# Optimization experiments

Hardware: AMD Instinct MI355X
Metric: run time of the kernel (lower is better)

The kernel has to match this reference:

```python
import jax, jax.numpy as jnp
import numpy as np

N, E = 50000, 800000
IN_FEAT = OUT_FEAT = 128
EMB = 3
K = 3  # k_order + 1
BN_EPS = 1e-5


def setup_inputs() -> dict:
    key = jax.random.key(0)
    ks = jax.random.split(key, 12)
    feature = jax.random.normal(ks[0], (N, IN_FEAT), jnp.float32)
    coords = jax.random.normal(ks[1], (N, EMB), jnp.float32)
    src = jax.random.randint(ks[2], (E,), 0, N, jnp.int32)
    dst = jax.random.randint(ks[3], (E,), 0, N, jnp.int32)
    order = jax.random.randint(ks[4], (E,), 0, K, jnp.int32)
    # xavier_normal_ on [K, in, out]: torch treats last two dims as (fan_in, fan_out)
    std_lin = float(np.sqrt(2.0 / (IN_FEAT + OUT_FEAT)))
    linear = jax.random.normal(ks[5], (K, IN_FEAT, OUT_FEAT), jnp.float32) * std_lin
    # attention_layer: Linear(EMB, OUT_FEAT, bias=False); store as [EMB, OUT_FEAT]
    lim_att = float(1.0 / np.sqrt(EMB))
    attW = jax.random.uniform(ks[6], (EMB, OUT_FEAT), jnp.float32, -lim_att, lim_att)
    lim_mlp = float(1.0 / np.sqrt(OUT_FEAT))
    mlp_w = jax.random.uniform(ks[7], (OUT_FEAT, OUT_FEAT), jnp.float32, -lim_mlp, lim_mlp)
    mlp_b = jax.random.uniform(ks[8], (OUT_FEAT,), jnp.float32, -lim_mlp, lim_mlp)
    bn_gamma = jnp.ones((OUT_FEAT,), jnp.float32)
    bn_beta = jnp.zeros((OUT_FEAT,), jnp.float32)
    return {"feature": feature, "coords": coords, "src": src, "dst": dst,
            "order": order, "linear": linear, "attW": attW,
            "mlp_w": mlp_w, "mlp_b": mlp_b, "bn_gamma": bn_gamma, "bn_beta": bn_beta}


def reference(feature, coords, src, dst, order, linear, attW, mlp_w, mlp_b, bn_gamma, bn_beta):
    n = feature.shape[0]
    # --- edge attention: dot(attention_layer(c_src - c_dst), h_src) ---
    dc = coords[src] - coords[dst]                      # [E, EMB]
    att = jnp.sum((dc @ attW) * feature[src], axis=1)   # [E]
    invdist = 1.0 / (jnp.sum(dc * dc, axis=1) + 1.0)    # [E], 1/(||dc||^2 + 1)
    # --- messages: per-edge weight selection linear[order] @ h_src ---
    # msg depends only on (src node, order): precompute per-order node transforms
    xk = jnp.einsum('ni,kio->kno', feature, linear)     # [K, N, OUT]
    msg = xk[order, src]                                # [E, OUT]
    # --- segment softmax over incoming edges of dst ---
    m = jax.ops.segment_max(att, dst, num_segments=n)   # [N]
    ex = jnp.exp(att - m[dst])                          # [E]
    denom = jax.ops.segment_sum(ex, dst, num_segments=n)
    d_g = denom[dst]
    alpha = ex / jnp.where(d_g > 0, d_g, 1.0)
    # --- weighted scatter-add aggregation ---
    w = (alpha * invdist)[:, None]                      # [E, 1]
    h = jax.ops.segment_sum(w * msg, dst, num_segments=n)  # [N, OUT]
    # --- mlp: Linear -> ReLU -> BatchNorm1d (training-mode batch stats) ---
    y = jax.nn.relu(h @ mlp_w.T + mlp_b)
    mean = jnp.mean(y, axis=0)
    var = jnp.var(y, axis=0)  # biased, matches torch BN normalization
    y = (y - mean) * jax.lax.rsqrt(var + BN_EPS) * bn_gamma + bn_beta
    return y
```

## Files before the change

kernel.cpp:

```cpp
#include <hip/hip_runtime.h>

#define N_NODES 50000
#define E_EDGES 800000
#define FEAT    128
#define KORD    3
#define BN_EPS  1e-5f
#define NB1     49
#define NBUK    49
#define BCAP    20480
#define NSHARD  16
#define NSEG    32
#define NWB_BLKS 12500
#define NZERO   54368

typedef __fp16 f16x2 __attribute__((ext_vector_type(2)));
typedef __fp16 f16x8 __attribute__((ext_vector_type(8)));
typedef __attribute__((ext_vector_type(4))) float f32x4;

__device__ __forceinline__ unsigned h2u(f16x2 h) { union { f16x2 h; unsigned u; } c; c.h = h; return c.u; }
__device__ __forceinline__ f16x2 u2h(unsigned u) { union { unsigned u; f16x2 h; } c; c.u = u; return c.h; }

__device__ __forceinline__ void gload16(const void* g, void* l) {
    __builtin_amdgcn_global_load_lds(
        (const __attribute__((address_space(1))) unsigned int*)g,
        (__attribute__((address_space(3))) unsigned int*)l, 16, 0, 0);
}

__global__ void g_cast(const float* __restrict__ feat,
                       const float* __restrict__ coords,
                       const float* __restrict__ attW,
                       const float* __restrict__ W,
                       const float* __restrict__ L,
                       __fp16* __restrict__ fh,
                       float4* __restrict__ pk,
                       __fp16* __restrict__ GT,
                       int* __restrict__ zbase) {
    __shared__ float wrow[FEAT];
    const int gtid = blockIdx.x * 256 + threadIdx.x;
    if (gtid < NZERO) zbase[gtid] = 0;
    if (blockIdx.x >= NWB_BLKS) {
        const int o = blockIdx.x - NWB_BLKS;
        const int i = threadIdx.x;
        if (i < FEAT) wrow[i] = W[o * FEAT + i];
        __syncthreads();
        if (i < FEAT) {
            #pragma unroll
            for (int k = 0; k < KORD; ++k) {
                const float* lp = L + ((size_t)k * FEAT + i) * FEAT;
                float acc = 0.f;
                #pragma unroll 8
                for (int j = 0; j < FEAT; ++j) acc = fmaf(lp[j], wrow[j], acc);
                GT[(size_t)o * 384 + k * FEAT + i] = (__fp16)acc;
            }
        }
        return;
    }
    const int node = gtid >> 6;
    const int lane = threadIdx.x & 63;
    if (node >= N_NODES) return;
    const float2 f = *(const float2*)(feat + (size_t)node * FEAT + lane * 2);
    *(f16x2*)(fh + (size_t)node * FEAT + lane * 2) = __builtin_amdgcn_cvt_pkrtz(f.x, f.y);
    float gg[3];
    #pragma unroll
    for (int j = 0; j < 3; ++j) {
        float p = f.x * attW[j * FEAT + lane * 2] + f.y * attW[j * FEAT + lane * 2 + 1];
        #pragma unroll
        for (int off = 32; off; off >>= 1) p += __shfl_xor(p, off);
        gg[j] = p;
    }
    if (lane == 0) {
        const float c0 = coords[node * 3 + 0], c1 = coords[node * 3 + 1], c2 = coords[node * 3 + 2];
        pk[2 * node]     = make_float4(c0, c1, c2, gg[0]);
        pk[2 * node + 1] = make_float4(gg[1], gg[2], 0.f, 0.f);
    }
}

__global__ __launch_bounds__(256)
void bucketA(const int* __restrict__ src, const int* __restrict__ dst,
             const int* __restrict__ order,
             int* __restrict__ cnt, int* __restrict__ gcur, int2* __restrict__ bbuf) {
    __shared__ int lcnt[4][NBUK];
    __shared__ int wbase[4][NBUK];
    const int tid = threadIdx.x;
    const int wid = tid >> 6;
    if (tid < NBUK) {
        lcnt[0][tid] = 0; lcnt[1][tid] = 0; lcnt[2][tid] = 0; lcnt[3][tid] = 0;
    }
    __syncthreads();
    const int e0 = blockIdx.x * 2048;
    int b[8], r[8], so[8], dd[8];
    #pragma unroll
    for (int i = 0; i < 8; ++i) {
        const int e = e0 + i * 256 + tid;
        if (e < E_EDGES) {
            dd[i] = dst[e];
            so[i] = (order[e] << 16) | src[e];
            b[i] = dd[i] >> 10;
            r[i] = atomicAdd(&lcnt[wid][b[i]], 1);
            atomicAdd(cnt + dd[i], 1);
        } else b[i] = -1;
    }
    __syncthreads();
    if (tid < NBUK) {
        const int w0 = lcnt[0][tid], w1 = lcnt[1][tid], w2 = lcnt[2][tid], w3 = lcnt[3][tid];
        const int base = atomicAdd(gcur + tid, w0 + w1 + w2 + w3);
        wbase[0][tid] = base;
        wbase[1][tid] = base + w0;
        wbase[2][tid] = base + w0 + w1;
        wbase[3][tid] = base + w0 + w1 + w2;
    }
    __syncthreads();
    #pragma unroll
    for (int i = 0; i < 8; ++i)
        if (b[i] >= 0)
            bbuf[(size_t)b[i] * BCAP + wbase[wid][b[i]] + r[i]] = make_int2(so[i], dd[i]);
}

__global__ __launch_bounds__(256)
void scan1(const int* __restrict__ cnt, int* __restrict__ rowptr, int* __restrict__ bsum) {
    __shared__ int lds[256];
    const int b = blockIdx.x, t = threadIdx.x;
    const int base = b * 1024 + t * 4;
    int v[4];
    #pragma unroll
    for (int i = 0; i < 4; ++i) v[i] = (base + i < N_NODES) ? cnt[base + i] : 0;
    lds[t] = v[0] + v[1] + v[2] + v[3];
    __syncthreads();
    for (int off = 1; off < 256; off <<= 1) {
        const int u = (t >= off) ? lds[t - off] : 0;
        __syncthreads();
        lds[t] += u;
        __syncthreads();
    }
    int excl = t ? lds[t - 1] : 0;
    if (t == 255) bsum[b] = lds[255];
    #pragma unroll
    for (int i = 0; i < 4; ++i) {
        if (base + i < N_NODES) rowptr[base + i] = excl;
        excl += v[i];
    }
}

__global__ void scan3(int* __restrict__ rowptr, int* __restrict__ cursor,
                      const int* __restrict__ bsum) {
    __shared__ int boff_s[64];
    const int t = threadIdx.x;
    if (t < 64) {
        const int v = (t < NB1) ? bsum[t] : 0;
        int incl = v;
        #pragma unroll
        for (int off = 1; off < 64; off <<= 1) {
            const int u = __shfl_up(incl, off);
            if (t >= off) incl += u;
        }
        boff_s[t] = incl - v;
    }
    __syncthreads();
    const int i = blockIdx.x * 256 + t;
    if (i < N_NODES) {
        const int v = rowptr[i] + boff_s[i >> 10];
        rowptr[i] = v;
        cursor[i] = v;
    }
    if (i == 0) rowptr[N_NODES] = E_EDGES;
}

__global__ void bucketB(const int* __restrict__ gcur, const int2* __restrict__ bbuf,
                        const float4* __restrict__ pk,
                        int* __restrict__ cursor, int4* __restrict__ edata) {
    const int b = blockIdx.x / NSEG;
    const int seg = blockIdx.x % NSEG;
    const int n = gcur[b];
    const int lo = (int)((long)n * seg / NSEG), hi = (int)((long)n * (seg + 1) / NSEG);
    for (int i = lo + (int)threadIdx.x; i < hi; i += 256) {
        const int2 ent = bbuf[(size_t)b * BCAP + i];
        const int s = ent.x & 0xFFFF;
        const int d = ent.y;
        const float4 a0 = pk[2 * s], a1 = pk[2 * s + 1], c0 = pk[2 * d];
        const float dx = a0.x - c0.x, dy = a0.y - c0.y, dz = a0.z - c0.z;
        const float att  = dx * a0.w + dy * a1.x + dz * a1.y;
        const float invd = 1.f / (dx * dx + dy * dy + dz * dz + 1.f);
        const int pos = atomicAdd(cursor + d, 1);
        edata[pos] = make_int4(ent.x, __float_as_int(att), __float_as_int(invd), 0);
    }
}

__global__ void segagg(const int4* __restrict__ edata,
                       const int* __restrict__ rowptr,
                       const __fp16* __restrict__ fh,
                       __fp16* __restrict__ agg) {
    __shared__ uint4 stash[4][64];
    const int node = (blockIdx.x * blockDim.x + threadIdx.x) >> 6;
    const int lane = threadIdx.x & 63;
    const int wid  = threadIdx.x >> 6;
    if (node >= N_NODES) return;
    const int beg = rowptr[node], end = rowptr[node + 1];

    int4 e0c = make_int4(0, 0xFF800000, 0, 0);
    float m = -1e30f, s = 0.f;
    int nch = 0;
    for (int cb = beg; cb < end; cb += 64, ++nch) {
        const int p = cb + lane;
        float a = -1e30f;
        if (p < end) {
            const int4 e = edata[p];
            a = __int_as_float(e.y);
            if (nch == 0) e0c = e;
        }
        const float mn = fmaxf(m, a);
        s = s * __expf(m - mn) + ((p < end) ? __expf(a - mn) : 0.f);
        m = mn;
    }
    #pragma unroll
    for (int off = 32; off; off >>= 1) {
        const float mo = __shfl_xor(m, off), so_ = __shfl_xor(s, off);
        const float mn = fmaxf(m, mo);
        s = s * __expf(m - mn) + so_ * __expf(mo - mn);
        m = mn;
    }
    const float inv_s = s > 0.f ? 1.f / s : 0.f;

    const int grp = lane >> 4;
    const int fl  = lane & 15;
    f16x2 ac[3][4];
    #pragma unroll
    for (int o = 0; o < 3; ++o)
        #pragma unroll
        for (int q = 0; q < 4; ++q) ac[o][q] = (f16x2){0, 0};

    int ch = 0;
    for (int cb = beg; cb < end; cb += 64, ++ch) {
        const int p = cb + lane;
        float wl = 0.f; int so = 0;
        if (p < end) {
            const int4 e = (ch == 0) ? e0c : edata[p];
            wl = __expf(__int_as_float(e.y) - m) * inv_s * __int_as_float(e.z);
            so = e.x;
        }
        const int k = so >> 16;
        const __fp16 wh = (__fp16)wl;
        f16x2 w2; w2.x = wh; w2.y = wh;
        const unsigned uw = h2u(w2);
        stash[wid][lane] = make_uint4(k == 0 ? uw : 0u, k == 1 ? uw : 0u,
                                      k == 2 ? uw : 0u, (unsigned)(so & 0xFFFF));
        const int ne = min(64, end - cb);
        const uint4* st = stash[wid];
        for (int t = 0; t < ne; t += 8) {
            const uint4 e1 = st[t + grp];
            const uint4 e2 = st[t + 4 + grp];
            const uint4 v1 = *(const uint4*)(fh + ((size_t)e1.w << 7) + fl * 8);
            const uint4 v2 = *(const uint4*)(fh + ((size_t)e2.w << 7) + fl * 8);
            {
                const f16x2 w0 = u2h(e1.x), w1 = u2h(e1.y), w2v = u2h(e1.z);
                const f16x2 va = u2h(v1.x), vb = u2h(v1.y), vc = u2h(v1.z), vd = u2h(v1.w);
                ac[0][0] = __builtin_elementwise_fma(va, w0, ac[0][0]);
                ac[0][1] = __builtin_elementwise_fma(vb, w0, ac[0][1]);
                ac[0][2] = __builtin_elementwise_fma(vc, w0, ac[0][2]);
                ac[0][3] = __builtin_elementwise_fma(vd, w0, ac[0][3]);
                ac[1][0] = __builtin_elementwise_fma(va, w1, ac[1][0]);
                ac[1][1] = __builtin_elementwise_fma(vb, w1, ac[1][1]);
                ac[1][2] = __builtin_elementwise_fma(vc, w1, ac[1][2]);
                ac[1][3] = __builtin_elementwise_fma(vd, w1, ac[1][3]);
                ac[2][0] = __builtin_elementwise_fma(va, w2v, ac[2][0]);
                ac[2][1] = __builtin_elementwise_fma(vb, w2v, ac[2][1]);
                ac[2][2] = __builtin_elementwise_fma(vc, w2v, ac[2][2]);
                ac[2][3] = __builtin_elementwise_fma(vd, w2v, ac[2][3]);
            }
            {
                const f16x2 w0 = u2h(e2.x), w1 = u2h(e2.y), w2v = u2h(e2.z);
                const f16x2 va = u2h(v2.x), vb = u2h(v2.y), vc = u2h(v2.z), vd = u2h(v2.w);
                ac[0][0] = __builtin_elementwise_fma(va, w0, ac[0][0]);
                ac[0][1] = __builtin_elementwise_fma(vb, w0, ac[0][1]);
                ac[0][2] = __builtin_elementwise_fma(vc, w0, ac[0][2]);
                ac[0][3] = __builtin_elementwise_fma(vd, w0, ac[0][3]);
                ac[1][0] = __builtin_elementwise_fma(va, w1, ac[1][0]);
                ac[1][1] = __builtin_elementwise_fma(vb, w1, ac[1][1]);
                ac[1][2] = __builtin_elementwise_fma(vc, w1, ac[1][2]);
                ac[1][3] = __builtin_elementwise_fma(vd, w1, ac[1][3]);
                ac[2][0] = __builtin_elementwise_fma(va, w2v, ac[2][0]);
                ac[2][1] = __builtin_elementwise_fma(vb, w2v, ac[2][1]);
                ac[2][2] = __builtin_elementwise_fma(vc, w2v, ac[2][2]);
                ac[2][3] = __builtin_elementwise_fma(vd, w2v, ac[2][3]);
            }
        }
    }
    #pragma unroll
    for (int o = 0; o < 3; ++o)
        #pragma unroll
        for (int q = 0; q < 4; ++q) {
            ac[o][q] = ac[o][q] + u2h(__shfl_xor((int)h2u(ac[o][q]), 16));
            ac[o][q] = ac[o][q] + u2h(__shfl_xor((int)h2u(ac[o][q]), 32));
        }
    if (lane < 16) {
        __fp16* row = agg + (size_t)node * 384 + fl * 8;
        *(uint4*)(row)       = make_uint4(h2u(ac[0][0]), h2u(ac[0][1]), h2u(ac[0][2]), h2u(ac[0][3]));
        *(uint4*)(row + 128) = make_uint4(h2u(ac[1][0]), h2u(ac[1][1]), h2u(ac[1][2]), h2u(ac[1][3]));
        *(uint4*)(row + 256) = make_uint4(h2u(ac[2][0]), h2u(ac[2][1]), h2u(ac[2][2]), h2u(ac[2][3]));
    }
}

__global__ __launch_bounds__(256)
void mlp_gemm(const __fp16* __restrict__ agg, const __fp16* __restrict__ GT,
              float* __restrict__ out, int M,
              const float* __restrict__ bias, float* __restrict__ sbuf) {
    __shared__ char smem[49152];
    const int m0 = blockIdx.x * 64;
    const int tid = threadIdx.x;
    const int wave = tid >> 6, lane = tid & 63;
    const int wm0 = wave * 16;
    const int lrow = lane & 15;
    const int kg = lane >> 4;
    const int srow = lane >> 3;
    const int schunk = lane & 7;

    auto STAGE = [&](int buf, int kc) {
        char* base = smem + buf * 24576;
        #pragma unroll
        for (int j = 0; j < 2; ++j) {
            const int rl = wave * 16 + j * 8 + srow;
            const int rg = min(m0 + rl, M - 1);
            gload16(agg + (size_t)rg * 384 + kc * 64 + ((schunk ^ (rl & 7)) << 3),
                    base + (wave * 16 + j * 8) * 128);
        }
        #pragma unroll
        for (int j = 0; j < 4; ++j) {
            const int rl = wave * 32 + j * 8 + srow;
            gload16(GT + (size_t)rl * 384 + kc * 64 + ((schunk ^ (rl & 7)) << 3),
                    base + 8192 + (wave * 32 + j * 8) * 128);
        }
    };

    f32x4 acc[8];
    #pragma unroll
    for (int b = 0; b < 8; ++b) acc[b] = (f32x4){0.f, 0.f, 0.f, 0.f};

    STAGE(0, 0);
    __syncthreads();

    for (int kc = 0; kc < 6; ++kc) {
        const int buf = kc & 1;
        if (kc < 5) STAGE(buf ^ 1, kc + 1);
        const char* Ab = smem + buf * 24576;
        const char* Bb = Ab + 8192;
        f16x8 afr[2];
        #pragma unroll
        for (int ks = 0; ks < 2; ++ks) {
            const int row = wm0 + lrow;
            afr[ks] = *(const f16x8*)(Ab + row * 128 + (((ks * 4 + kg) ^ (row & 7)) << 4));
        }
        #pragma unroll
        for (int nf = 0; nf < 8; ++nf) {
            #pragma unroll
            for (int ks = 0; ks < 2; ++ks) {
                const int row = nf * 16 + lrow;
                f16x8 bfr = *(const f16x8*)(Bb + row * 128 + (((ks * 4 + kg) ^ (row & 7)) << 4));
                acc[nf] = __builtin_amdgcn_mfma_f32_16x16x32_f16(afr[ks], bfr, acc[nf], 0, 0, 0);
            }
        }
        __syncthreads();
    }

    float s[8], s2[8], bv[8];
    #pragma unroll
    for (int nf = 0; nf < 8; ++nf) { s[nf] = 0.f; s2[nf] = 0.f; bv[nf] = bias[nf * 16 + lrow]; }
    #pragma unroll
    for (int nf = 0; nf < 8; ++nf)
        #pragma unroll
        for (int rg = 0; rg < 4; ++rg) {
            const int row = m0 + wm0 + kg * 4 + rg;
            if (row < M) {
                const float v = fmaxf(acc[nf][rg] + bv[nf], 0.f);
                out[(size_t)row * FEAT + nf * 16 + lrow] = v;
                s[nf] += v;
                s2[nf] = fmaf(v, v, s2[nf]);
            }
        }
    #pragma unroll
    for (int nf = 0; nf < 8; ++nf) {
        s[nf]  += __shfl_xor(s[nf], 16);  s[nf]  += __shfl_xor(s[nf], 32);
        s2[nf] += __shfl_xor(s2[nf], 16); s2[nf] += __shfl_xor(s2[nf], 32);
    }
    __syncthreads();
    float* red = (float*)smem;
    if (lane < 16) {
        #pragma unroll
        for (int nf = 0; nf < 8; ++nf) {
            red[wave * 256 + nf * 16 + lane]       = s[nf];
            red[wave * 256 + 128 + nf * 16 + lane] = s2[nf];
        }
    }
    __syncthreads();
    if (tid < 128) {
        const float ss = red[tid] + red[256 + tid] + red[512 + tid] + red[768 + tid];
        const float qq = red[128 + tid] + red[384 + tid] + red[640 + tid] + red[896 + tid];
        float* sb = sbuf + (blockIdx.x & (NSHARD - 1)) * 256;
        atomicAdd(sb + tid, ss);
        atomicAdd(sb + FEAT + tid, qq);
    }
}

__global__ void normalize(float* __restrict__ y, const float* __restrict__ sbuf,
                          const float* __restrict__ gamma, const float* __restrict__ beta) {
    __shared__ float sc_s[FEAT], sh_s[FEAT];
    const int t = threadIdx.x;
    if (t < FEAT) {
        float ssum = 0.f, qsum = 0.f;
        #pragma unroll
        for (int sh = 0; sh < NSHARD; ++sh) {
            ssum += sbuf[sh * 256 + t];
            qsum += sbuf[sh * 256 + 128 + t];
        }
        const float mean = ssum / (float)N_NODES;
        const float var  = qsum / (float)N_NODES - mean * mean;
        const float sc   = gamma[t] * rsqrtf(var + BN_EPS);
        sc_s[t] = sc;
        sh_s[t] = beta[t] - mean * sc;
    }
    __syncthreads();
    const int idx = blockIdx.x * blockDim.x + t;
    const int o4 = (idx & 31) * 4;
    float4 v = *(float4*)(y + (size_t)idx * 4);
    const float4 sc = *(const float4*)(sc_s + o4);
    const float4 sh = *(const float4*)(sh_s + o4);
    v.x = fmaf(v.x, sc.x, sh.x);
    v.y = fmaf(v.y, sc.y, sh.y);
    v.z = fmaf(v.z, sc.z, sh.z);
    v.w = fmaf(v.w, sc.w, sh.w);
    *(float4*)(y + (size_t)idx * 4) = v;
}

extern "C" void kernel_launch(void* const* d_in, const int* in_sizes, int n_in,
                              void* d_out, int out_size, void* d_ws, size_t ws_size,
                              hipStream_t stream) {
    const float* feature = (const float*)d_in[0];
    const float* coords  = (const float*)d_in[1];
    const int*   src     = (const int*)d_in[2];
    const int*   dst     = (const int*)d_in[3];
    const int*   order   = (const int*)d_in[4];
    const float* linear  = (const float*)d_in[5];
    const float* attW    = (const float*)d_in[6];
    const float* mlp_w   = (const float*)d_in[7];
    const float* mlp_b   = (const float*)d_in[8];
    const float* gamma   = (const float*)d_in[9];
    const float* beta    = (const float*)d_in[10];
    float* out = (float*)d_out;

    char* p = (char*)d_ws;
    __fp16* fh           = (__fp16*)p;  p += (size_t)N_NODES * FEAT * 2;
    __fp16* agg          = (__fp16*)p;  p += (size_t)N_NODES * 384 * 2;
    __fp16* GT           = (__fp16*)p;  p += (size_t)FEAT * 384 * 2;
    float4* pk           = (float4*)p;  p += (size_t)N_NODES * 32;
    int4*  edata         = (int4*)p;    p += (size_t)E_EDGES * 16;
    int2*  bbuf          = (int2*)p;    p += (size_t)NBUK * BCAP * 8;
    int*   cnt           = (int*)p;     p += 200064;
    float* sbuf          = (float*)p;   p += NSHARD * 256 * 4;
    int*   gcur          = (int*)p;     p += 1024;
    int*   rowptr        = (int*)p;     p += 200064;
    int*   cursor        = (int*)p;     p += 200064;
    int*   bsum          = (int*)p;     p += 256;

    const int MB = (N_NODES + 63) / 64;
    const int AB = (E_EDGES + 2047) / 2048;

    g_cast<<<NWB_BLKS + FEAT, 256, 0, stream>>>(feature, coords, attW,
                                                mlp_w, linear, fh, pk, GT, cnt);

    bucketA<<<AB, 256, 0, stream>>>(src, dst, order, cnt, gcur, bbuf);
    scan1<<<NB1, 256, 0, stream>>>(cnt, rowptr, bsum);
    scan3<<<(N_NODES + 255) / 256, 256, 0, stream>>>(rowptr, cursor, bsum);
    bucketB<<<NBUK * NSEG, 256, 0, stream>>>(gcur, bbuf, pk, cursor, edata);

    segagg<<<NWB_BLKS, 256, 0, stream>>>(edata, rowptr, fh, agg);

    mlp_gemm<<<MB, 256, 0, stream>>>(agg, GT, out, N_NODES, mlp_b, sbuf);
    normalize<<<(N_NODES * 32) / 256, 256, 0, stream>>>(out, sbuf, gamma, beta);
}
```

Baseline: 172.1 us.

## Compute per-node degree histogram from buckets and fuse scans into one kernel

Stops bucketA from issuing a global atomicAdd per edge into a degree array. A new hist2 kernel builds the per-node histogram for each 1024-node bucket in LDS from the already bucketed edges, scans it, and adds the bucket offset taken from a scan over the bucket counts. This replaces two scan kernels and shrinks the zeroing region because the cnt array is gone. The cost is a second read pass over bbuf, and only 49 blocks with heavy LDS atomics, so parallelism in this stage is low.

Result: faster. 162.6 us (-5.5%).

```diff
diff --git a/kernel.cpp b/kernel.cpp
--- a/kernel.cpp
+++ b/kernel.cpp
@@ -5,13 +5,12 @@
 #define FEAT    128
 #define KORD    3
 #define BN_EPS  1e-5f
-#define NB1     49
 #define NBUK    49
 #define BCAP    20480
 #define NSHARD  16
 #define NSEG    32
 #define NWB_BLKS 12500
-#define NZERO   54368
+#define NZERO   4352
 
 typedef __fp16 f16x2 __attribute__((ext_vector_type(2)));
 typedef __fp16 f16x8 __attribute__((ext_vector_type(8)));
@@ -78,7 +77,7 @@
 __global__ __launch_bounds__(256)
 void bucketA(const int* __restrict__ src, const int* __restrict__ dst,
              const int* __restrict__ order,
-             int* __restrict__ cnt, int* __restrict__ gcur, int2* __restrict__ bbuf) {
+             int* __restrict__ gcur, int2* __restrict__ bbuf) {
     __shared__ int lcnt[4][NBUK];
     __shared__ int wbase[4][NBUK];
     const int tid = threadIdx.x;
@@ -97,7 +96,6 @@
             so[i] = (order[e] << 16) | src[e];
             b[i] = dd[i] >> 10;
             r[i] = atomicAdd(&lcnt[wid][b[i]], 1);
-            atomicAdd(cnt + dd[i], 1);
         } else b[i] = -1;
     }
     __syncthreads();
@@ -117,52 +115,50 @@
 }
 
 __global__ __launch_bounds__(256)
-void scan1(const int* __restrict__ cnt, int* __restrict__ rowptr, int* __restrict__ bsum) {
-    __shared__ int lds[256];
-    const int b = blockIdx.x, t = threadIdx.x;
-    const int base = b * 1024 + t * 4;
-    int v[4];
-    #pragma unroll
-    for (int i = 0; i < 4; ++i) v[i] = (base + i < N_NODES) ? cnt[base + i] : 0;
-    lds[t] = v[0] + v[1] + v[2] + v[3];
-    __syncthreads();
-    for (int off = 1; off < 256; off <<= 1) {
-        const int u = (t >= off) ? lds[t - off] : 0;
-        __syncthreads();
-        lds[t] += u;
-        __syncthreads();
-    }
-    int excl = t ? lds[t - 1] : 0;
-    if (t == 255) bsum[b] = lds[255];
-    #pragma unroll
-    for (int i = 0; i < 4; ++i) {
-        if (base + i < N_NODES) rowptr[base + i] = excl;
-        excl += v[i];
-    }
-}
-
-__global__ void scan3(int* __restrict__ rowptr, int* __restrict__ cursor,
-                      const int* __restrict__ bsum) {
-    __shared__ int boff_s[64];
+void hist2(const int* __restrict__ gcur, const int2* __restrict__ bbuf,
+           int* __restrict__ rowptr, int* __restrict__ cursor) {
+    __shared__ int lhist[1024];
+    __shared__ int lscan[256];
+    __shared__ int boff_s;
+    const int b = blockIdx.x;
     const int t = threadIdx.x;
+    #pragma unroll
+    for (int i = 0; i < 4; ++i) lhist[t + i * 256] = 0;
+    __syncthreads();
+    const int n = gcur[b];
+    const int base = b << 10;
+    for (int i = t; i < n; i += 256)
+        atomicAdd(&lhist[bbuf[(size_t)b * BCAP + i].y - base], 1);
+    __syncthreads();
     if (t < 64) {
-        const int v = (t < NB1) ? bsum[t] : 0;
+        const int v = (t < NBUK) ? gcur[t] : 0;
         int incl = v;
         #pragma unroll
         for (int off = 1; off < 64; off <<= 1) {
             const int u = __shfl_up(incl, off);
             if (t >= off) incl += u;
         }
-        boff_s[t] = incl - v;
-    }
-    __syncthreads();
-    const int i = blockIdx.x * 256 + t;
-    if (i < N_NODES) {
-        const int v = rowptr[i] + boff_s[i >> 10];
-        rowptr[i] = v;
-        cursor[i] = v;
-    }
-    if (i == 0) rowptr[N_NODES] = E_EDGES;
+        if (t == b) boff_s = incl - v;
+    }
+    int v[4];
+    #pragma unroll
+    for (int i = 0; i < 4; ++i) v[i] = lhist[t * 4 + i];
+    lscan[t] = v[0] + v[1] + v[2] + v[3];
+    __syncthreads();
+    for (int off = 1; off < 256; off <<= 1) {
+        const int u = (t >= off) ? lscan[t - off] : 0;
+        __syncthreads();
+        lscan[t] += u;
+        __syncthreads();
+    }
+    int excl = (t ? lscan[t - 1] : 0) + boff_s;
+    #pragma unroll
+    for (int i = 0; i < 4; ++i) {
+        const int node = base + t * 4 + i;
+        if (node < N_NODES) { rowptr[node] = excl; cursor[node] = excl; }
+        excl += v[i];
+    }
+    if (b == 0 && t == 0) rowptr[N_NODES] = E_EDGES;
 }
 
 __global__ void bucketB(const int* __restrict__ gcur, const int2* __restrict__ bbuf,
@@ -452,22 +448,19 @@
     float4* pk           = (float4*)p;  p += (size_t)N_NODES * 32;
     int4*  edata         = (int4*)p;    p += (size_t)E_EDGES * 16;
     int2*  bbuf          = (int2*)p;    p += (size_t)NBUK * BCAP * 8;
-    int*   cnt           = (int*)p;     p += 200064;
     float* sbuf          = (float*)p;   p += NSHARD * 256 * 4;
     int*   gcur          = (int*)p;     p += 1024;
     int*   rowptr        = (int*)p;     p += 200064;
     int*   cursor        = (int*)p;     p += 200064;
-    int*   bsum          = (int*)p;     p += 256;
 
     const int MB = (N_NODES + 63) / 64;
     const int AB = (E_EDGES + 2047) / 2048;
 
     g_cast<<<NWB_BLKS + FEAT, 256, 0, stream>>>(feature, coords, attW,
-                                                mlp_w, linear, fh, pk, GT, cnt);
-
-    bucketA<<<AB, 256, 0, stream>>>(src, dst, order, cnt, gcur, bbuf);
-    scan1<<<NB1, 256, 0, stream>>>(cnt, rowptr, bsum);
-    scan3<<<(N_NODES + 255) / 256, 256, 0, stream>>>(rowptr, cursor, bsum);
+                                                mlp_w, linear, fh, pk, GT, (int*)sbuf);
+
+    bucketA<<<AB, 256, 0, stream>>>(src, dst, order, gcur, bbuf);
+    hist2<<<NBUK, 256, 0, stream>>>(gcur, bbuf, rowptr, cursor);
     bucketB<<<NBUK * NSEG, 256, 0, stream>>>(gcur, bbuf, pk, cursor, edata);
 
     segagg<<<NWB_BLKS, 256, 0, stream>>>(edata, rowptr, fh, agg);
```
